# Kernel optimization log

Hardware: AMD Instinct MI355X
Metric: run time of the kernel (lower is better)

Reference implementation:

```python
import jax, jax.numpy as jnp
import numpy as np

COUT, CIN = 1024, 1024  # self.shape = (cout, cin) in the torch module
NNZ = 131072


def setup_inputs() -> dict:
    key = jax.random.key(0)
    k_x, k_v, k_r, k_c = jax.random.split(key, 4)
    x = jax.random.normal(k_x, (4, 4096, CIN), dtype=jnp.float32)
    values = jax.random.normal(k_v, (NNZ,), dtype=jnp.float32)
    rows = jax.random.randint(k_r, (NNZ,), 0, COUT, dtype=jnp.int32)
    cols = jax.random.randint(k_c, (NNZ,), 0, CIN, dtype=jnp.int32)
    indices = jnp.stack([rows, cols], axis=0)  # [2, nnz], integer-valued
    return {"x": x, "values": values, "indices": indices}


def reference(x, values, indices):
    # torch: sparse_coo_tensor(indices, values, (cout, cin)).coalesce();
    # coalescing sums duplicate (row, col) entries -> scatter-add densify.
    rows, cols = indices[0], indices[1]
    W = jnp.zeros((COUT, CIN), dtype=values.dtype).at[rows, cols].add(values)
    # 3D path: out[b, l, co] = sum_ci W[co, ci] * x[b, l, ci]
    return jnp.einsum('blc,oc->blo', x, W)
```

## Files before the change

### kernel.cpp

```cpp
#include <hip/hip_runtime.h>
#include <cstdint>
#include <cstddef>

#define CIN  1024
#define COUT 1024

typedef __attribute__((ext_vector_type(8))) short bf16x8;
typedef __attribute__((ext_vector_type(4))) float f32x4;

__device__ __forceinline__ unsigned short f2bf(float f) {
    union { float f; unsigned int i; } v;
    v.f = f;
    unsigned int u = v.i;
    u += 0x7FFFu + ((u >> 16) & 1u);
    return (unsigned short)(u >> 16);
}

__global__ void zero_f32(float4* __restrict__ p) {
    p[blockIdx.x * 256 + threadIdx.x] = float4{0.f, 0.f, 0.f, 0.f};
}

__global__ void scatter_add(const float* __restrict__ vals,
                            const int* __restrict__ rows,
                            const int* __restrict__ cols,
                            float* __restrict__ W, int nnz) {
    int i = blockIdx.x * 256 + threadIdx.x;
    if (i < nnz) {
        atomicAdd(W + (size_t)rows[i] * CIN + cols[i], vals[i]);
    }
}

__global__ void cvt_bf16_bulk(const float* __restrict__ src, unsigned short* __restrict__ dst) {
    size_t i = ((size_t)blockIdx.x * 256 + threadIdx.x) * 8;
    float4 v0 = *(const float4*)(src + i);
    float4 v1 = *(const float4*)(src + i + 4);
    union { bf16x8 v; unsigned short u[8]; } w;
    w.u[0] = f2bf(v0.x); w.u[1] = f2bf(v0.y); w.u[2] = f2bf(v0.z); w.u[3] = f2bf(v0.w);
    w.u[4] = f2bf(v1.x); w.u[5] = f2bf(v1.y); w.u[6] = f2bf(v1.z); w.u[7] = f2bf(v1.w);
    *(bf16x8*)(dst + i) = w.v;
}


#define GLD16(SRC_, DST_)                                                     \
  __builtin_amdgcn_global_load_lds(                                           \
      (const __attribute__((address_space(1))) void*)(SRC_),                  \
      (__attribute__((address_space(3))) void*)(DST_), 16, 0, 0)

#define STAGE_A(BUF_, HALF_, KT_) do {                                        \
    GLD16(pa + (size_t)((HALF_) * 128)      * CIN + (size_t)(KT_) * 64,       \
          As + (BUF_) * 16384 + ((HALF_) * 128) * 64 + tid8);                 \
    GLD16(pa + (size_t)((HALF_) * 128 + 64) * CIN + (size_t)(KT_) * 64,       \
          As + (BUF_) * 16384 + ((HALF_) * 128 + 64) * 64 + tid8);            \
  } while (0)

#define STAGE_B(BUF_, HALF_, KT_) do {                                        \
    GLD16(pb + (size_t)((HALF_) * 128)      * CIN + (size_t)(KT_) * 64,       \
          Bs + (BUF_) * 16384 + ((HALF_) * 128) * 64 + tid8);                 \
    GLD16(pb + (size_t)((HALF_) * 128 + 64) * CIN + (size_t)(KT_) * 64,       \
          Bs + (BUF_) * 16384 + ((HALF_) * 128 + 64) * 64 + tid8);            \
  } while (0)

#define LOAD_A(BUF_, QA_) do {                                                \
    const unsigned short* ab_ = As + (BUF_) * 16384 + ((QA_) * 128 + wm64) * 64; \
    _Pragma("unroll")                                                         \
    for (int ks_ = 0; ks_ < 2; ++ks_) {                                       \
      const int cx_ = ((ks_ * 4 + quad) ^ s7) * 8;                            \
      _Pragma("unroll")                                                       \
      for (int mf_ = 0; mf_ < 4; ++mf_)                                       \
        af[ks_][mf_] = *(const bf16x8*)(ab_ + (mf_ * 16 + l16) * 64 + cx_);   \
    }                                                                         \
  } while (0)

#define LOAD_B(BUF_, QB_, DST_) do {                                          \
    const unsigned short* bb_ = Bs + (BUF_) * 16384 + ((QB_) * 128 + wn32) * 64; \
    _Pragma("unroll")                                                         \
    for (int ks_ = 0; ks_ < 2; ++ks_) {                                       \
      const int cx_ = ((ks_ * 4 + quad) ^ s7) * 8;                            \
      _Pragma("unroll")                                                       \
      for (int nf_ = 0; nf_ < 2; ++nf_)                                       \
        DST_[ks_][nf_] = *(const bf16x8*)(bb_ + (nf_ * 16 + l16) * 64 + cx_); \
    }                                                                         \
  } while (0)

#define MFMA_Q(QA_, QB_, BF_)                                                 \
    _Pragma("unroll")                                                         \
    for (int ks_ = 0; ks_ < 2; ++ks_)                                         \
      _Pragma("unroll")                                                       \
      for (int mf_ = 0; mf_ < 4; ++mf_)                                       \
        _Pragma("unroll")                                                     \
        for (int nf_ = 0; nf_ < 2; ++nf_)                                     \
          acc[QA_][QB_][mf_][nf_] = __builtin_amdgcn_mfma_f32_16x16x32_bf16(  \
              af[ks_][mf_], BF_[ks_][nf_], acc[QA_][QB_][mf_][nf_], 0, 0, 0)

#define SYNC_PRE() do {                                                       \
    __builtin_amdgcn_s_barrier();                                             \
    asm volatile("s_waitcnt lgkmcnt(0)" ::: "memory");                        \
    __builtin_amdgcn_sched_barrier(0);                                        \
    __builtin_amdgcn_s_setprio(1);                                            \
  } while (0)

#define SYNC_POST() __builtin_amdgcn_s_setprio(0)

__global__ __launch_bounds__(512, 2) void gemm_8ph(
    const unsigned short* __restrict__ A,
    const unsigned short* __restrict__ B,
    float* __restrict__ C,
    int M) {
    (void)M;
    constexpr int K = CIN;

    __shared__ __align__(16) unsigned short As[2 * 16384];
    __shared__ __align__(16) unsigned short Bs[2 * 16384];

    const int tid  = threadIdx.x;
    const int lane = tid & 63;
    const int w    = tid >> 6;
    const int quad = lane >> 4;
    const int l16  = lane & 15;
    const int s7   = l16 & 7;
    const int wm64 = (w >> 2) * 64;
    const int wn32 = (w & 3) * 32;

    const int rowA0 = blockIdx.x * 256;
    const int rowB0 = blockIdx.y * 256;

    const int stg_row = tid >> 3;
    const int c_data  = (tid & 7) ^ (stg_row & 7);
    const int tid8    = tid * 8;
    const unsigned short* pa = A + (size_t)(rowA0 + stg_row) * K + c_data * 8;
    const unsigned short* pb = B + (size_t)(rowB0 + stg_row) * K + c_data * 8;

    f32x4 acc[2][2][4][2] = {};

    STAGE_A(0, 0, 0); STAGE_B(0, 0, 0); STAGE_B(0, 1, 0); STAGE_A(0, 1, 0);
    STAGE_A(1, 0, 1); STAGE_B(1, 0, 1);
    asm volatile("s_waitcnt vmcnt(4)" ::: "memory");
    __builtin_amdgcn_s_barrier();

#pragma unroll 1
    for (int i = 0; i < 8; ++i) {
        const int  k1 = 2 * i + 1;
        const int  k2 = 2 * i + 2;
        const int  k3 = 2 * i + 3;
        const bool nl = (i < 7);

        bf16x8 af[2][4];
        bf16x8 bf0[2][2], bf1[2][2];

        LOAD_A(0, 0); LOAD_B(0, 0, bf0);
        STAGE_B(1, 1, k1);
        SYNC_PRE(); MFMA_Q(0, 0, bf0); SYNC_POST();
        __builtin_amdgcn_s_barrier();
        LOAD_B(0, 1, bf1);
        STAGE_A(1, 1, k1);
        SYNC_PRE(); MFMA_Q(0, 1, bf1); SYNC_POST();
        __builtin_amdgcn_s_barrier();
        LOAD_A(0, 1);
        if (nl) STAGE_A(0, 0, k2);
        SYNC_PRE(); MFMA_Q(1, 0, bf0); SYNC_POST();
        __builtin_amdgcn_s_barrier();
        if (nl) STAGE_B(0, 0, k2);
        SYNC_PRE(); MFMA_Q(1, 1, bf1); SYNC_POST();
        if (nl) { asm volatile("s_waitcnt vmcnt(4)" ::: "memory"); }
        else    { asm volatile("s_waitcnt vmcnt(0)" ::: "memory"); }
        __builtin_amdgcn_s_barrier();

        LOAD_A(1, 0); LOAD_B(1, 0, bf0);
        if (nl) STAGE_B(0, 1, k2);
        SYNC_PRE(); MFMA_Q(0, 0, bf0); SYNC_POST();
        __builtin_amdgcn_s_barrier();
        LOAD_B(1, 1, bf1);
        if (nl) STAGE_A(0, 1, k2);
        SYNC_PRE(); MFMA_Q(0, 1, bf1); SYNC_POST();
        __builtin_amdgcn_s_barrier();
        LOAD_A(1, 1);
        if (nl) STAGE_A(1, 0, k3);
        SYNC_PRE(); MFMA_Q(1, 0, bf0); SYNC_POST();
        __builtin_amdgcn_s_barrier();
        if (nl) STAGE_B(1, 0, k3);
        SYNC_PRE(); MFMA_Q(1, 1, bf1); SYNC_POST();
        if (nl) { asm volatile("s_waitcnt vmcnt(4)" ::: "memory"); }
        __builtin_amdgcn_s_barrier();
    }

#pragma unroll
    for (int qa = 0; qa < 2; ++qa)
#pragma unroll
        for (int qb = 0; qb < 2; ++qb)
#pragma unroll
            for (int mf = 0; mf < 4; ++mf)
#pragma unroll
                for (int nf = 0; nf < 2; ++nf) {
                    const int row0 = rowA0 + qa * 128 + wm64 + mf * 16 + quad * 4;
                    float* cp = C + (size_t)row0 * COUT
                                  + rowB0 + qb * 128 + wn32 + nf * 16 + l16;
#pragma unroll
                    for (int r = 0; r < 4; ++r)
                        cp[(size_t)r * COUT] = acc[qa][qb][mf][nf][r];
                }
}

extern "C" void kernel_launch(void* const* d_in, const int* in_sizes, int n_in,
                              void* d_out, int out_size, void* d_ws, size_t ws_size,
                              hipStream_t stream) {
    const float* x    = (const float*)d_in[0];
    const float* vals = (const float*)d_in[1];
    const int*   idx  = (const int*)d_in[2];

    float* out = (float*)d_out;

    const int nnz = in_sizes[2] / 2;
    const int M   = in_sizes[0] / CIN;

    const size_t wf_bytes = (size_t)COUT * CIN * sizeof(float);
    const size_t wb_bytes = (size_t)COUT * CIN * sizeof(unsigned short);

    float*          Wf = (float*)d_ws;
    unsigned short* Wb = (unsigned short*)((char*)d_ws + wf_bytes);
    unsigned short* Xb = (unsigned short*)((char*)d_ws + wf_bytes + wb_bytes);

    zero_f32<<<dim3(COUT * CIN / (256 * 4)), dim3(256), 0, stream>>>((float4*)Wf);
    scatter_add<<<dim3((nnz + 255) / 256), dim3(256), 0, stream>>>(vals, idx, idx + nnz, Wf, nnz);
    cvt_bf16_bulk<<<dim3(COUT * CIN / (256 * 8)), dim3(256), 0, stream>>>(Wf, Wb);
    cvt_bf16_bulk<<<dim3((unsigned)((size_t)M * CIN / (256 * 8))), dim3(256), 0, stream>>>(x, Xb);
    gemm_8ph<<<dim3(M / 256, COUT / 256), dim3(512), 0, stream>>>(Xb, Wb, out, M);
}
```

Before: 161.3 us.

## Fuse densify, conversions and GEMM into one cooperative kernel with grid syncs

Replaces the five separate launches (zero, scatter-add, two bf16 conversions, GEMM) with a single cooperative kernel. Grid-stride loops handle the prep stages, separated by grid.sync(), and the GEMM tiles then map from a flattened 1D block index. The goal is to remove launch overhead and inter-kernel gaps. In exchange the prep phases run on only 256 blocks, grid-wide barriers are added, and the whole grid (256 blocks at 2 per CU) must be co-resident.

```diff
diff --git a/kernel.cpp b/kernel.cpp
--- a/kernel.cpp
+++ b/kernel.cpp
@@ -1,6 +1,9 @@
 #include <hip/hip_runtime.h>
+#include <hip/hip_cooperative_groups.h>
 #include <cstdint>
 #include <cstddef>
+
+namespace cg = cooperative_groups;
 
 #define CIN  1024
 #define COUT 1024
@@ -16,28 +19,14 @@
     return (unsigned short)(u >> 16);
 }
 
-__global__ void zero_f32(float4* __restrict__ p) {
-    p[blockIdx.x * 256 + threadIdx.x] = float4{0.f, 0.f, 0.f, 0.f};
-}
-
-__global__ void scatter_add(const float* __restrict__ vals,
-                            const int* __restrict__ rows,
-                            const int* __restrict__ cols,
-                            float* __restrict__ W, int nnz) {
-    int i = blockIdx.x * 256 + threadIdx.x;
-    if (i < nnz) {
-        atomicAdd(W + (size_t)rows[i] * CIN + cols[i], vals[i]);
-    }
-}
-
-__global__ void cvt_bf16_bulk(const float* __restrict__ src, unsigned short* __restrict__ dst) {
-    size_t i = ((size_t)blockIdx.x * 256 + threadIdx.x) * 8;
-    float4 v0 = *(const float4*)(src + i);
-    float4 v1 = *(const float4*)(src + i + 4);
+__device__ __forceinline__ void cvt8(const float* __restrict__ s,
+                                     unsigned short* __restrict__ d) {
+    float4 v0 = *(const float4*)s;
+    float4 v1 = *(const float4*)(s + 4);
     union { bf16x8 v; unsigned short u[8]; } w;
     w.u[0] = f2bf(v0.x); w.u[1] = f2bf(v0.y); w.u[2] = f2bf(v0.z); w.u[3] = f2bf(v0.w);
     w.u[4] = f2bf(v1.x); w.u[5] = f2bf(v1.y); w.u[6] = f2bf(v1.z); w.u[7] = f2bf(v1.w);
-    *(bf16x8*)(dst + i) = w.v;
+    *(bf16x8*)d = w.v;
 }
 
 
@@ -101,18 +90,44 @@
 
 #define SYNC_POST() __builtin_amdgcn_s_setprio(0)
 
-__global__ __launch_bounds__(512, 2) void gemm_8ph(
-    const unsigned short* __restrict__ A,
-    const unsigned short* __restrict__ B,
+__global__ __launch_bounds__(512, 2) void fused_all(
+    const float* __restrict__ x,
+    const float* __restrict__ vals,
+    const int* __restrict__ rows,
+    const int* __restrict__ cols,
+    float* __restrict__ Wf,
+    unsigned short* __restrict__ Wb,
+    unsigned short* __restrict__ Xb,
     float* __restrict__ C,
-    int M) {
-    (void)M;
+    int M, int nnz) {
+    cg::grid_group grid = cg::this_grid();
+
+    const int tid = threadIdx.x;
+    const unsigned gtid = blockIdx.x * 512u + (unsigned)tid;
+    const unsigned gsz  = gridDim.x * 512u;
+
+    for (unsigned i = gtid; i < COUT * CIN / 4; i += gsz)
+        ((float4*)Wf)[i] = float4{0.f, 0.f, 0.f, 0.f};
+    const size_t xchunks = (size_t)M * CIN / 8;
+    for (size_t i = gtid; i < xchunks; i += gsz)
+        cvt8(x + i * 8, Xb + i * 8);
+    grid.sync();
+
+    for (unsigned i = gtid; i < (unsigned)nnz; i += gsz)
+        atomicAdd(Wf + (size_t)rows[i] * CIN + cols[i], vals[i]);
+    grid.sync();
+
+    for (unsigned i = gtid; i < COUT * CIN / 8; i += gsz)
+        cvt8(Wf + (size_t)i * 8, Wb + (size_t)i * 8);
+    grid.sync();
+
     constexpr int K = CIN;
-
     __shared__ __align__(16) unsigned short As[2 * 16384];
     __shared__ __align__(16) unsigned short Bs[2 * 16384];
 
-    const int tid  = threadIdx.x;
+    const int nbx  = M / 256;
+    const int bx   = (int)blockIdx.x % nbx;
+    const int by   = (int)blockIdx.x / nbx;
     const int lane = tid & 63;
     const int w    = tid >> 6;
     const int quad = lane >> 4;
@@ -121,14 +136,14 @@
     const int wm64 = (w >> 2) * 64;
     const int wn32 = (w & 3) * 32;
 
-    const int rowA0 = blockIdx.x * 256;
-    const int rowB0 = blockIdx.y * 256;
+    const int rowA0 = bx * 256;
+    const int rowB0 = by * 256;
 
     const int stg_row = tid >> 3;
     const int c_data  = (tid & 7) ^ (stg_row & 7);
     const int tid8    = tid * 8;
-    const unsigned short* pa = A + (size_t)(rowA0 + stg_row) * K + c_data * 8;
-    const unsigned short* pb = B + (size_t)(rowB0 + stg_row) * K + c_data * 8;
+    const unsigned short* pa = Xb + (size_t)(rowA0 + stg_row) * K + c_data * 8;
+    const unsigned short* pb = Wb + (size_t)(rowB0 + stg_row) * K + c_data * 8;
 
     f32x4 acc[2][2][4][2] = {};
 
@@ -151,14 +166,17 @@
         STAGE_B(1, 1, k1);
         SYNC_PRE(); MFMA_Q(0, 0, bf0); SYNC_POST();
         __builtin_amdgcn_s_barrier();
+
         LOAD_B(0, 1, bf1);
         STAGE_A(1, 1, k1);
         SYNC_PRE(); MFMA_Q(0, 1, bf1); SYNC_POST();
         __builtin_amdgcn_s_barrier();
+
         LOAD_A(0, 1);
         if (nl) STAGE_A(0, 0, k2);
         SYNC_PRE(); MFMA_Q(1, 0, bf0); SYNC_POST();
         __builtin_amdgcn_s_barrier();
+
         if (nl) STAGE_B(0, 0, k2);
         SYNC_PRE(); MFMA_Q(1, 1, bf1); SYNC_POST();
         if (nl) { asm volatile("s_waitcnt vmcnt(4)" ::: "memory"); }
@@ -169,14 +187,17 @@
         if (nl) STAGE_B(0, 1, k2);
         SYNC_PRE(); MFMA_Q(0, 0, bf0); SYNC_POST();
         __builtin_amdgcn_s_barrier();
+
         LOAD_B(1, 1, bf1);
         if (nl) STAGE_A(0, 1, k2);
         SYNC_PRE(); MFMA_Q(0, 1, bf1); SYNC_POST();
         __builtin_amdgcn_s_barrier();
+
         LOAD_A(1, 1);
         if (nl) STAGE_A(1, 0, k3);
         SYNC_PRE(); MFMA_Q(1, 0, bf0); SYNC_POST();
         __builtin_amdgcn_s_barrier();
+
         if (nl) STAGE_B(1, 0, k3);
         SYNC_PRE(); MFMA_Q(1, 1, bf1); SYNC_POST();
         if (nl) { asm volatile("s_waitcnt vmcnt(4)" ::: "memory"); }
@@ -209,8 +230,8 @@
 
     float* out = (float*)d_out;
 
-    const int nnz = in_sizes[2] / 2;
-    const int M   = in_sizes[0] / CIN;
+    int nnz = in_sizes[2] / 2;
+    int M   = in_sizes[0] / CIN;
 
     const size_t wf_bytes = (size_t)COUT * CIN * sizeof(float);
     const size_t wb_bytes = (size_t)COUT * CIN * sizeof(unsigned short);
@@ -219,9 +240,15 @@
     unsigned short* Wb = (unsigned short*)((char*)d_ws + wf_bytes);
     unsigned short* Xb = (unsigned short*)((char*)d_ws + wf_bytes + wb_bytes);
 
-    zero_f32<<<dim3(COUT * CIN / (256 * 4)), dim3(256), 0, stream>>>((float4*)Wf);
-    scatter_add<<<dim3((nnz + 255) / 256), dim3(256), 0, stream>>>(vals, idx, idx + nnz, Wf, nnz);
-    cvt_bf16_bulk<<<dim3(COUT * CIN / (256 * 8)), dim3(256), 0, stream>>>(Wf, Wb);
-    cvt_bf16_bulk<<<dim3((unsigned)((size_t)M * CIN / (256 * 8))), dim3(256), 0, stream>>>(x, Xb);
-    gemm_8ph<<<dim3(M / 256, COUT / 256), dim3(512), 0, stream>>>(Xb, Wb, out, M);
-}
+    const int* rowsP = idx;
+    const int* colsP = idx + nnz;
+
+    void* args[] = {
+        (void*)&x, (void*)&vals, (void*)&rowsP, (void*)&colsP,
+        (void*)&Wf, (void*)&Wb, (void*)&Xb, (void*)&out,
+        (void*)&M, (void*)&nnz
+    };
+    const unsigned nblk = (unsigned)((M / 256) * (COUT / 256));
+    hipLaunchCooperativeKernel((const void*)fused_all, dim3(nblk), dim3(512),
+                               args, 0, stream);
+}
```

Measured after the change: 251.2 us. 55.8% more time.

## Fuse fp32-to-bf16 conversion of x into the GEMM A-operand staging

Applied to the files above, without the earlier changes.

Drops the separate bulk kernel that converted x to bf16. The GEMM now loads fp32 x tiles into registers, converts them to bf16, and writes them to LDS itself, interleaved with the existing B async loads and MFMA phases. This removes a full write and re-read of the bf16 copy of x through global memory. The cost is that each of the four column-tile blocks sharing a row tile reads twice as many bytes of x and converts it again, and the conversion adds VALU work, register pressure and reordered vmcnt waits to the pipeline.

```diff
diff --git a/kernel.cpp b/kernel.cpp
--- a/kernel.cpp
+++ b/kernel.cpp
@@ -46,18 +46,32 @@
       (const __attribute__((address_space(1))) void*)(SRC_),                  \
       (__attribute__((address_space(3))) void*)(DST_), 16, 0, 0)
 
-#define STAGE_A(BUF_, HALF_, KT_) do {                                        \
-    GLD16(pa + (size_t)((HALF_) * 128)      * CIN + (size_t)(KT_) * 64,       \
-          As + (BUF_) * 16384 + ((HALF_) * 128) * 64 + tid8);                 \
-    GLD16(pa + (size_t)((HALF_) * 128 + 64) * CIN + (size_t)(KT_) * 64,       \
-          As + (BUF_) * 16384 + ((HALF_) * 128 + 64) * 64 + tid8);            \
-  } while (0)
-
 #define STAGE_B(BUF_, HALF_, KT_) do {                                        \
     GLD16(pb + (size_t)((HALF_) * 128)      * CIN + (size_t)(KT_) * 64,       \
           Bs + (BUF_) * 16384 + ((HALF_) * 128) * 64 + tid8);                 \
     GLD16(pb + (size_t)((HALF_) * 128 + 64) * CIN + (size_t)(KT_) * 64,       \
           Bs + (BUF_) * 16384 + ((HALF_) * 128 + 64) * 64 + tid8);            \
+  } while (0)
+
+#define A_ISSUE(HALF_, KT_) do {                                              \
+    const float* s0_ = pxa + (size_t)((HALF_) * 128) * CIN + (size_t)(KT_) * 64; \
+    const float* s1_ = s0_ + (size_t)64 * CIN;                                \
+    ar0 = *(const float4*)s0_;  ar1 = *(const float4*)(s0_ + 4);              \
+    ar2 = *(const float4*)s1_;  ar3 = *(const float4*)(s1_ + 4);              \
+  } while (0)
+
+#define A_WRITE(BUF_, HALF_) do {                                             \
+    union { bf16x8 v; unsigned short u[8]; } w0_, w1_;                        \
+    w0_.u[0] = f2bf(ar0.x); w0_.u[1] = f2bf(ar0.y);                           \
+    w0_.u[2] = f2bf(ar0.z); w0_.u[3] = f2bf(ar0.w);                           \
+    w0_.u[4] = f2bf(ar1.x); w0_.u[5] = f2bf(ar1.y);                           \
+    w0_.u[6] = f2bf(ar1.z); w0_.u[7] = f2bf(ar1.w);                           \
+    w1_.u[0] = f2bf(ar2.x); w1_.u[1] = f2bf(ar2.y);                           \
+    w1_.u[2] = f2bf(ar2.z); w1_.u[3] = f2bf(ar2.w);                           \
+    w1_.u[4] = f2bf(ar3.x); w1_.u[5] = f2bf(ar3.y);                           \
+    w1_.u[6] = f2bf(ar3.z); w1_.u[7] = f2bf(ar3.w);                           \
+    *(bf16x8*)(As + (BUF_) * 16384 + ((HALF_) * 128) * 64 + tid8)      = w0_.v; \
+    *(bf16x8*)(As + (BUF_) * 16384 + ((HALF_) * 128 + 64) * 64 + tid8) = w1_.v; \
   } while (0)
 
 #define LOAD_A(BUF_, QA_) do {                                                \
@@ -101,8 +115,8 @@
 
 #define SYNC_POST() __builtin_amdgcn_s_setprio(0)
 
-__global__ __launch_bounds__(512, 2) void gemm_8ph(
-    const unsigned short* __restrict__ A,
+__global__ __launch_bounds__(512, 2) void gemm_8ph_fused(
+    const float* __restrict__ X,
     const unsigned short* __restrict__ B,
     float* __restrict__ C,
     int M) {
@@ -127,14 +141,18 @@
     const int stg_row = tid >> 3;
     const int c_data  = (tid & 7) ^ (stg_row & 7);
     const int tid8    = tid * 8;
-    const unsigned short* pa = A + (size_t)(rowA0 + stg_row) * K + c_data * 8;
-    const unsigned short* pb = B + (size_t)(rowB0 + stg_row) * K + c_data * 8;
+    const float* pxa          = X + (size_t)(rowA0 + stg_row) * K + c_data * 8;
+    const unsigned short* pb  = B + (size_t)(rowB0 + stg_row) * K + c_data * 8;
 
     f32x4 acc[2][2][4][2] = {};
-
-    STAGE_A(0, 0, 0); STAGE_B(0, 0, 0); STAGE_B(0, 1, 0); STAGE_A(0, 1, 0);
-    STAGE_A(1, 0, 1); STAGE_B(1, 0, 1);
-    asm volatile("s_waitcnt vmcnt(4)" ::: "memory");
+    float4 ar0, ar1, ar2, ar3;
+
+    STAGE_B(0, 0, 0); STAGE_B(0, 1, 0);
+    A_ISSUE(0, 0);  A_WRITE(0, 0);
+    A_ISSUE(1, 0);  A_WRITE(0, 1);
+    A_ISSUE(0, 1);  A_WRITE(1, 0);
+    STAGE_B(1, 0, 1);
+    asm volatile("s_waitcnt lgkmcnt(0)" ::: "memory");
     __builtin_amdgcn_s_barrier();
 
 #pragma unroll 1
@@ -148,38 +166,39 @@
         bf16x8 bf0[2][2], bf1[2][2];
 
         LOAD_A(0, 0); LOAD_B(0, 0, bf0);
+        A_ISSUE(1, k1);
         STAGE_B(1, 1, k1);
         SYNC_PRE(); MFMA_Q(0, 0, bf0); SYNC_POST();
         __builtin_amdgcn_s_barrier();
+        A_WRITE(1, 1);
         LOAD_B(0, 1, bf1);
-        STAGE_A(1, 1, k1);
         SYNC_PRE(); MFMA_Q(0, 1, bf1); SYNC_POST();
         __builtin_amdgcn_s_barrier();
         LOAD_A(0, 1);
-        if (nl) STAGE_A(0, 0, k2);
+        if (nl) { A_ISSUE(0, k2); STAGE_B(0, 0, k2); }
         SYNC_PRE(); MFMA_Q(1, 0, bf0); SYNC_POST();
         __builtin_amdgcn_s_barrier();
-        if (nl) STAGE_B(0, 0, k2);
+        if (nl) A_WRITE(0, 0);
         SYNC_PRE(); MFMA_Q(1, 1, bf1); SYNC_POST();
-        if (nl) { asm volatile("s_waitcnt vmcnt(4)" ::: "memory"); }
+        if (nl) { asm volatile("s_waitcnt vmcnt(2)" ::: "memory"); }
         else    { asm volatile("s_waitcnt vmcnt(0)" ::: "memory"); }
         __builtin_amdgcn_s_barrier();
 
         LOAD_A(1, 0); LOAD_B(1, 0, bf0);
-        if (nl) STAGE_B(0, 1, k2);
+        if (nl) { A_ISSUE(1, k2); STAGE_B(0, 1, k2); }
         SYNC_PRE(); MFMA_Q(0, 0, bf0); SYNC_POST();
         __builtin_amdgcn_s_barrier();
+        if (nl) A_WRITE(0, 1);
         LOAD_B(1, 1, bf1);
-        if (nl) STAGE_A(0, 1, k2);
         SYNC_PRE(); MFMA_Q(0, 1, bf1); SYNC_POST();
         __builtin_amdgcn_s_barrier();
         LOAD_A(1, 1);
-        if (nl) STAGE_A(1, 0, k3);
+        if (nl) { A_ISSUE(0, k3); STAGE_B(1, 0, k3); }
         SYNC_PRE(); MFMA_Q(1, 0, bf0); SYNC_POST();
         __builtin_amdgcn_s_barrier();
-        if (nl) STAGE_B(1, 0, k3);
+        if (nl) A_WRITE(1, 0);
         SYNC_PRE(); MFMA_Q(1, 1, bf1); SYNC_POST();
-        if (nl) { asm volatile("s_waitcnt vmcnt(4)" ::: "memory"); }
+        if (nl) { asm volatile("s_waitcnt vmcnt(2)" ::: "memory"); }
         __builtin_amdgcn_s_barrier();
     }
 
@@ -213,15 +232,12 @@
     const int M   = in_sizes[0] / CIN;
 
     const size_t wf_bytes = (size_t)COUT * CIN * sizeof(float);
-    const size_t wb_bytes = (size_t)COUT * CIN * sizeof(unsigned short);
 
     float*          Wf = (float*)d_ws;
     unsigned short* Wb = (unsigned short*)((char*)d_ws + wf_bytes);
-    unsigned short* Xb = (unsigned short*)((char*)d_ws + wf_bytes + wb_bytes);
 
     zero_f32<<<dim3(COUT * CIN / (256 * 4)), dim3(256), 0, stream>>>((float4*)Wf);
     scatter_add<<<dim3((nnz + 255) / 256), dim3(256), 0, stream>>>(vals, idx, idx + nnz, Wf, nnz);
     cvt_bf16_bulk<<<dim3(COUT * CIN / (256 * 8)), dim3(256), 0, stream>>>(Wf, Wb);
-    cvt_bf16_bulk<<<dim3((unsigned)((size_t)M * CIN / (256 * 8))), dim3(256), 0, stream>>>(x, Xb);
-    gemm_8ph<<<dim3(M / 256, COUT / 256), dim3(512), 0, stream>>>(Xb, Wb, out, M);
-}
+    gemm_8ph_fused<<<dim3(M / 256, COUT / 256), dim3(512), 0, stream>>>(x, Wb, out, M);
+}
```

After: 181.0 us. 12.2% more time.

## Fuse scatter-add with x conversion and peel last GEMM iteration to overlap stores

Applied to the files above, without the earlier changes.

Merges the sparse scatter-add kernel and the x fp32-to-bf16 conversion into one launch by splitting the grid by block index, removing one kernel launch and letting the two independent jobs run concurrently. The GEMM's final K iteration is peeled out of the loop so the per-phase conditionals disappear. In the peeled tail, each accumulator quadrant is written to C right after its last MFMA, overlapping epilogue stores with the remaining math. The tail drops some barriers and reorders LDS reads, which needs care for correctness and may change register pressure.

```diff
diff --git a/kernel.cpp b/kernel.cpp
--- a/kernel.cpp
+++ b/kernel.cpp
@@ -16,28 +16,39 @@
     return (unsigned short)(u >> 16);
 }
 
-__global__ void zero_f32(float4* __restrict__ p) {
-    p[blockIdx.x * 256 + threadIdx.x] = float4{0.f, 0.f, 0.f, 0.f};
-}
-
-__global__ void scatter_add(const float* __restrict__ vals,
-                            const int* __restrict__ rows,
-                            const int* __restrict__ cols,
-                            float* __restrict__ W, int nnz) {
-    int i = blockIdx.x * 256 + threadIdx.x;
-    if (i < nnz) {
-        atomicAdd(W + (size_t)rows[i] * CIN + cols[i], vals[i]);
-    }
-}
-
-__global__ void cvt_bf16_bulk(const float* __restrict__ src, unsigned short* __restrict__ dst) {
-    size_t i = ((size_t)blockIdx.x * 256 + threadIdx.x) * 8;
-    float4 v0 = *(const float4*)(src + i);
-    float4 v1 = *(const float4*)(src + i + 4);
+__device__ __forceinline__ void cvt8(const float* __restrict__ s,
+                                     unsigned short* __restrict__ d) {
+    float4 v0 = *(const float4*)s;
+    float4 v1 = *(const float4*)(s + 4);
     union { bf16x8 v; unsigned short u[8]; } w;
     w.u[0] = f2bf(v0.x); w.u[1] = f2bf(v0.y); w.u[2] = f2bf(v0.z); w.u[3] = f2bf(v0.w);
     w.u[4] = f2bf(v1.x); w.u[5] = f2bf(v1.y); w.u[6] = f2bf(v1.z); w.u[7] = f2bf(v1.w);
-    *(bf16x8*)(dst + i) = w.v;
+    *(bf16x8*)d = w.v;
+}
+
+__global__ void zero_f32(float4* __restrict__ p) {
+    p[blockIdx.x * 256 + threadIdx.x] = float4{0.f, 0.f, 0.f, 0.f};
+}
+
+__global__ void scatter_cvtx(const float* __restrict__ vals,
+                             const int* __restrict__ rows,
+                             const int* __restrict__ cols,
+                             float* __restrict__ W, int nnz, int nsb,
+                             const float* __restrict__ x,
+                             unsigned short* __restrict__ Xb) {
+    const int b = blockIdx.x;
+    if (b < nsb) {
+        const int i = b * 256 + threadIdx.x;
+        if (i < nnz) atomicAdd(W + (size_t)rows[i] * CIN + cols[i], vals[i]);
+    } else {
+        const size_t i = (((size_t)(b - nsb) * 256) + threadIdx.x) * 8;
+        cvt8(x + i, Xb + i);
+    }
+}
+
+__global__ void cvt_bf16_bulk(const float* __restrict__ src, unsigned short* __restrict__ dst) {
+    size_t i = ((size_t)blockIdx.x * 256 + threadIdx.x) * 8;
+    cvt8(src + i, dst + i);
 }
 
 
@@ -92,6 +103,20 @@
           acc[QA_][QB_][mf_][nf_] = __builtin_amdgcn_mfma_f32_16x16x32_bf16(  \
               af[ks_][mf_], BF_[ks_][nf_], acc[QA_][QB_][mf_][nf_], 0, 0, 0)
 
+#define WRITE_CQ(QA_, QB_) do {                                               \
+    _Pragma("unroll")                                                         \
+    for (int mf_ = 0; mf_ < 4; ++mf_)                                         \
+      _Pragma("unroll")                                                       \
+      for (int nf_ = 0; nf_ < 2; ++nf_) {                                     \
+        const int row0_ = rowA0 + (QA_) * 128 + wm64 + mf_ * 16 + quad * 4;   \
+        float* cp_ = C + (size_t)row0_ * COUT                                 \
+                       + rowB0 + (QB_) * 128 + wn32 + nf_ * 16 + l16;         \
+        _Pragma("unroll")                                                     \
+        for (int r_ = 0; r_ < 4; ++r_)                                        \
+            cp_[(size_t)r_ * COUT] = acc[QA_][QB_][mf_][nf_][r_];             \
+      }                                                                       \
+  } while (0)
+
 #define SYNC_PRE() do {                                                       \
     __builtin_amdgcn_s_barrier();                                             \
     asm volatile("s_waitcnt lgkmcnt(0)" ::: "memory");                        \
@@ -101,7 +126,12 @@
 
 #define SYNC_POST() __builtin_amdgcn_s_setprio(0)
 
-__global__ __launch_bounds__(512, 2) void gemm_8ph(
+#define WAIT_LGKM() do {                                                      \
+    asm volatile("s_waitcnt lgkmcnt(0)" ::: "memory");                        \
+    __builtin_amdgcn_sched_barrier(0);                                        \
+  } while (0)
+
+__global__ __launch_bounds__(512, 2) void gemm_8ph_peel(
     const unsigned short* __restrict__ A,
     const unsigned short* __restrict__ B,
     float* __restrict__ C,
@@ -138,11 +168,10 @@
     __builtin_amdgcn_s_barrier();
 
 #pragma unroll 1
-    for (int i = 0; i < 8; ++i) {
-        const int  k1 = 2 * i + 1;
-        const int  k2 = 2 * i + 2;
-        const int  k3 = 2 * i + 3;
-        const bool nl = (i < 7);
+    for (int i = 0; i < 7; ++i) {
+        const int k1 = 2 * i + 1;
+        const int k2 = 2 * i + 2;
+        const int k3 = 2 * i + 3;
 
         bf16x8 af[2][4];
         bf16x8 bf0[2][2], bf1[2][2];
@@ -151,53 +180,81 @@
         STAGE_B(1, 1, k1);
         SYNC_PRE(); MFMA_Q(0, 0, bf0); SYNC_POST();
         __builtin_amdgcn_s_barrier();
+
         LOAD_B(0, 1, bf1);
         STAGE_A(1, 1, k1);
         SYNC_PRE(); MFMA_Q(0, 1, bf1); SYNC_POST();
         __builtin_amdgcn_s_barrier();
+
         LOAD_A(0, 1);
-        if (nl) STAGE_A(0, 0, k2);
+        STAGE_A(0, 0, k2);
         SYNC_PRE(); MFMA_Q(1, 0, bf0); SYNC_POST();
         __builtin_amdgcn_s_barrier();
-        if (nl) STAGE_B(0, 0, k2);
+
+        STAGE_B(0, 0, k2);
         SYNC_PRE(); MFMA_Q(1, 1, bf1); SYNC_POST();
-        if (nl) { asm volatile("s_waitcnt vmcnt(4)" ::: "memory"); }
-        else    { asm volatile("s_waitcnt vmcnt(0)" ::: "memory"); }
+        asm volatile("s_waitcnt vmcnt(4)" ::: "memory");
         __builtin_amdgcn_s_barrier();
 
         LOAD_A(1, 0); LOAD_B(1, 0, bf0);
-        if (nl) STAGE_B(0, 1, k2);
+        STAGE_B(0, 1, k2);
         SYNC_PRE(); MFMA_Q(0, 0, bf0); SYNC_POST();
         __builtin_amdgcn_s_barrier();
+
         LOAD_B(1, 1, bf1);
-        if (nl) STAGE_A(0, 1, k2);
+        STAGE_A(0, 1, k2);
         SYNC_PRE(); MFMA_Q(0, 1, bf1); SYNC_POST();
         __builtin_amdgcn_s_barrier();
+
         LOAD_A(1, 1);
-        if (nl) STAGE_A(1, 0, k3);
+        STAGE_A(1, 0, k3);
         SYNC_PRE(); MFMA_Q(1, 0, bf0); SYNC_POST();
         __builtin_amdgcn_s_barrier();
-        if (nl) STAGE_B(1, 0, k3);
+
+        STAGE_B(1, 0, k3);
         SYNC_PRE(); MFMA_Q(1, 1, bf1); SYNC_POST();
-        if (nl) { asm volatile("s_waitcnt vmcnt(4)" ::: "memory"); }
+        asm volatile("s_waitcnt vmcnt(4)" ::: "memory");
         __builtin_amdgcn_s_barrier();
     }
 
-#pragma unroll
-    for (int qa = 0; qa < 2; ++qa)
-#pragma unroll
-        for (int qb = 0; qb < 2; ++qb)
-#pragma unroll
-            for (int mf = 0; mf < 4; ++mf)
-#pragma unroll
-                for (int nf = 0; nf < 2; ++nf) {
-                    const int row0 = rowA0 + qa * 128 + wm64 + mf * 16 + quad * 4;
-                    float* cp = C + (size_t)row0 * COUT
-                                  + rowB0 + qb * 128 + wn32 + nf * 16 + l16;
-#pragma unroll
-                    for (int r = 0; r < 4; ++r)
-                        cp[(size_t)r * COUT] = acc[qa][qb][mf][nf][r];
-                }
+    {
+        bf16x8 af[2][4];
+        bf16x8 bf0[2][2], bf1[2][2];
+
+        LOAD_A(0, 0); LOAD_B(0, 0, bf0);
+        STAGE_B(1, 1, 15);
+        SYNC_PRE(); MFMA_Q(0, 0, bf0); SYNC_POST();
+        __builtin_amdgcn_s_barrier();
+
+        LOAD_B(0, 1, bf1);
+        STAGE_A(1, 1, 15);
+        SYNC_PRE(); MFMA_Q(0, 1, bf1); SYNC_POST();
+        __builtin_amdgcn_s_barrier();
+
+        LOAD_A(0, 1);
+        SYNC_PRE(); MFMA_Q(1, 0, bf0); SYNC_POST();
+        __builtin_amdgcn_s_barrier();
+
+        SYNC_PRE(); MFMA_Q(1, 1, bf1); SYNC_POST();
+        asm volatile("s_waitcnt vmcnt(0)" ::: "memory");
+        __builtin_amdgcn_s_barrier();
+
+        LOAD_A(1, 0); LOAD_B(1, 0, bf0); LOAD_B(1, 1, bf1);
+        WAIT_LGKM();
+        __builtin_amdgcn_s_setprio(1); MFMA_Q(0, 0, bf0); __builtin_amdgcn_s_setprio(0);
+        WRITE_CQ(0, 0);
+
+        __builtin_amdgcn_s_setprio(1); MFMA_Q(0, 1, bf1); __builtin_amdgcn_s_setprio(0);
+        WRITE_CQ(0, 1);
+
+        LOAD_A(1, 1);
+        WAIT_LGKM();
+        __builtin_amdgcn_s_setprio(1); MFMA_Q(1, 0, bf0); __builtin_amdgcn_s_setprio(0);
+        WRITE_CQ(1, 0);
+
+        __builtin_amdgcn_s_setprio(1); MFMA_Q(1, 1, bf1); __builtin_amdgcn_s_setprio(0);
+        WRITE_CQ(1, 1);
+    }
 }
 
 extern "C" void kernel_launch(void* const* d_in, const int* in_sizes, int n_in,
@@ -219,9 +276,12 @@
     unsigned short* Wb = (unsigned short*)((char*)d_ws + wf_bytes);
     unsigned short* Xb = (unsigned short*)((char*)d_ws + wf_bytes + wb_bytes);
 
+    const int nsb = (nnz + 255) / 256;
+    const unsigned cvtx_blocks = (unsigned)((size_t)M * CIN / (256 * 8));
+
     zero_f32<<<dim3(COUT * CIN / (256 * 4)), dim3(256), 0, stream>>>((float4*)Wf);
-    scatter_add<<<dim3((nnz + 255) / 256), dim3(256), 0, stream>>>(vals, idx, idx + nnz, Wf, nnz);
+    scatter_cvtx<<<dim3((unsigned)nsb + cvtx_blocks), dim3(256), 0, stream>>>(
+        vals, idx, idx + nnz, Wf, nnz, nsb, x, Xb);
     cvt_bf16_bulk<<<dim3(COUT * CIN / (256 * 8)), dim3(256), 0, stream>>>(Wf, Wb);
-    cvt_bf16_bulk<<<dim3((unsigned)((size_t)M * CIN / (256 * 8))), dim3(256), 0, stream>>>(x, Xb);
-    gemm_8ph<<<dim3(M / 256, COUT / 256), dim3(512), 0, stream>>>(Xb, Wb, out, M);
-}
+    gemm_8ph_peel<<<dim3(M / 256, COUT / 256), dim3(512), 0, stream>>>(Xb, Wb, out, M);
+}
```

Result: faster. 155.4 us (-3.6%).
